# Performance work log

Measured on AMD Instinct MI355X. Metric: run time of the kernel, lower is better.

The kernel has to match this reference:

```python
import jax, jax.numpy as jnp
import numpy as np

B, N = 16, 286
EMB_DIM = 4
CLOUD_DIM = 4
NB = 3          # number_of_basis
HID = 150       # radial MLP hidden width
RADIUS = 3.0    # neighbor radius / max_radius of cosine basis
FF = 512


def sp5(x):
    # torch Softplus(beta=5)
    return jax.nn.softplus(5.0 * x) / 5.0


def cosine_basis(r):
    # e3nn CosineBasisModel embedding: cos^2 bumps on [0, RADIUS]
    centers = jnp.linspace(0.0, RADIUS, NB)
    step = centers[1] - centers[0]
    d = (r[..., None] - centers) / step                     # [B,N,N,NB]
    return jnp.cos(jnp.pi / 2 * d) ** 2 * (jnp.abs(d) < 1.0)


def cloud_conv(feats, dist, mask, ws, bs, dim_out):
    # radial MLP on pairwise distances -> per-pair [dim_out, dim_in] kernel (l=0 only)
    x = cosine_basis(dist)
    for w, b in zip(ws[:-1], bs[:-1]):
        x = sp5(x @ w + b)
    R = x @ ws[-1] + bs[-1]                                 # [B,N,N,dim_out*dim_in]
    b_, n_ = dist.shape[0], dist.shape[1]
    k = R.reshape(b_, n_, n_, dim_out, -1) * mask[..., None, None]
    nb = jnp.maximum(mask.sum(-1), 1.0)                     # neighbors per atom [B,N]
    out = jnp.einsum('zabij,zbj->zai', k, feats) / jnp.sqrt(nb)[..., None]
    return out


def setup_inputs() -> dict:
    key = jax.random.key(0)
    ks = jax.random.split(key, 32)
    xyz = jax.random.normal(ks[0], (B, N, 3), dtype=jnp.float32)
    Z = jax.random.randint(ks[1], (B, N), 0, 11)
    emb = jax.random.normal(ks[2], (11, EMB_DIM), dtype=jnp.float32)
    inp = {'xyz': xyz, 'Z': Z, 'emb': emb}
    # radial MLPs per cloud: 3 -> 150 -> 150 -> 150 -> dim_out*dim_in (=16)
    dims = [NB, HID, HID, HID, CLOUD_DIM * CLOUD_DIM]
    ki = 3
    for c in range(2):
        for l in range(4):
            w = jax.random.normal(ks[ki], (dims[l], dims[l + 1]), dtype=jnp.float32) / np.sqrt(dims[l])
            b = jnp.zeros((dims[l + 1],), dtype=jnp.float32)
            inp[f'c{c}_w{l}'] = w
            inp[f'c{c}_b{l}'] = b
            ki += 1
    cloud_out = CLOUD_DIM * 2  # cloud_dim * cloud_order^2 * nclouds = 8
    inp['fc_w'] = jax.random.normal(ks[ki], (cloud_out, FF), dtype=jnp.float32) / np.sqrt(cloud_out); ki += 1
    inp['fc_b'] = jnp.zeros((FF,), dtype=jnp.float32)
    inp['bn_g'] = jnp.ones((FF,), dtype=jnp.float32)
    inp['bn_b'] = jnp.zeros((FF,), dtype=jnp.float32)
    inp['out_w'] = jax.random.normal(ks[ki], (FF, 1), dtype=jnp.float32) / np.sqrt(FF); ki += 1
    inp['out_b'] = jnp.zeros((1,), dtype=jnp.float32)
    return inp


def reference(xyz, Z, emb,
              c0_w0, c0_b0, c0_w1, c0_b1, c0_w2, c0_b2, c0_w3, c0_b3,
              c1_w0, c1_b0, c1_w1, c1_b1, c1_w2, c1_b2, c1_w3, c1_b3,
              fc_w, fc_b, bn_g, bn_b, out_w, out_b):
    feats = emb[Z]                                          # [B,N,emb_dim]
    diff = xyz[:, :, None, :] - xyz[:, None, :, :]
    dist = jnp.sqrt(jnp.sum(diff * diff, -1) + 1e-12)       # [B,N,N]
    mask = (dist < RADIUS).astype(feats.dtype)
    f1 = cloud_conv(feats, dist, mask,
                    [c0_w0, c0_w1, c0_w2, c0_w3], [c0_b0, c0_b1, c0_b2, c0_b3], CLOUD_DIM)
    f2 = cloud_conv(f1, dist, mask,
                    [c1_w0, c1_w1, c1_w2, c1_w3], [c1_b0, c1_b1, c1_b2, c1_b3], CLOUD_DIM)
    feats_cat = jnp.concatenate([f1, f2], axis=2)           # [B,N,8]
    # lp_pool2d(norm=2, kernel=(N,1)) == L2 norm over atom dim
    pooled = jnp.sqrt(jnp.sum(feats_cat ** 2, axis=1))      # [B,8]
    h = jax.nn.softplus(pooled @ fc_w + fc_b)
    mean = h.mean(0)
    var = h.var(0)
    h = jax.nn.softplus((h - mean) / jnp.sqrt(var + 1e-5) * bn_g + bn_b)
    return jax.nn.sigmoid(h @ out_w + out_b)[:, 0]          # [B]
```

## Files before the change

kernel.cpp:

```cpp
#include <hip/hip_runtime.h>
#include <hip/hip_bf16.h>
#include <hip/hip_fp16.h>
#include <math.h>

#define B_SZ   16
#define N_ATOM 286
#define NT     1024
#define HIDW   150
#define FF_DIM 512
#define WPAD   152
#define WROWS  151

__device__ __forceinline__ float softplus_f(float x) {
  return fmaxf(x, 0.0f) + log1pf(expf(-fabsf(x)));
}
__device__ __forceinline__ float sp5_f(float x) {
  float t = 5.0f * x;
  return (fmaxf(t, 0.0f) + log1pf(expf(-fabsf(t)))) * 0.2f;
}

__global__ __launch_bounds__(256) void prep_kernel(
    const float* __restrict__ w1a, const float* __restrict__ b1a,
    const float* __restrict__ w2a, const float* __restrict__ b2a,
    const float* __restrict__ w1c, const float* __restrict__ b1c,
    const float* __restrict__ w2c, const float* __restrict__ b2c,
    float* __restrict__ Wp) {
  const int m = blockIdx.y;
  const float* W  = (m == 0) ? w1a : (m == 1) ? w2a : (m == 2) ? w1c : w2c;
  const float* Bb = (m == 0) ? b1a : (m == 1) ? b2a : (m == 2) ? b1c : b2c;
  int idx = blockIdx.x * 256 + threadIdx.x;
  if (idx < WROWS * WPAD) {
    int i = idx / WPAD, o = idx % WPAD;
    float v = 0.0f;
    if (o < HIDW) v = (i < HIDW) ? W[i * HIDW + o] : Bb[o];
    Wp[(size_t)m * WROWS * WPAD + idx] = v;
  }
}

__device__ __forceinline__ void hidden_layer_v2(
    const float* __restrict__ Wp,
    const float* __restrict__ src,
    float* __restrict__ dst,
    int jj, int e0) {
  const float4 bb = *(const float4*)(Wp + HIDW * WPAD + 4 * jj);
  float4 a0 = bb, a1 = bb;
  #pragma unroll 8
  for (int i = 0; i < HIDW; ++i) {
    float4 wv = *(const float4*)(Wp + i * WPAD + 4 * jj);
    float2 h  = *(const float2*)(src + i * 8 + e0);
    a0.x = __builtin_fmaf(h.x, wv.x, a0.x); a1.x = __builtin_fmaf(h.y, wv.x, a1.x);
    a0.y = __builtin_fmaf(h.x, wv.y, a0.y); a1.y = __builtin_fmaf(h.y, wv.y, a1.y);
    a0.z = __builtin_fmaf(h.x, wv.z, a0.z); a1.z = __builtin_fmaf(h.y, wv.z, a1.z);
    a0.w = __builtin_fmaf(h.x, wv.w, a0.w); a1.w = __builtin_fmaf(h.y, wv.w, a1.w);
  }
  *(float2*)(dst + (4 * jj + 0) * 8 + e0) = make_float2(sp5_f(a0.x), sp5_f(a1.x));
  *(float2*)(dst + (4 * jj + 1) * 8 + e0) = make_float2(sp5_f(a0.y), sp5_f(a1.y));
  *(float2*)(dst + (4 * jj + 2) * 8 + e0) = make_float2(sp5_f(a0.z), sp5_f(a1.z));
  *(float2*)(dst + (4 * jj + 3) * 8 + e0) = make_float2(sp5_f(a0.w), sp5_f(a1.w));
}

__global__ __launch_bounds__(256) void table_kernel(
    const float* __restrict__ a_w0, const float* __restrict__ a_b0,
    const float* __restrict__ a_w3, const float* __restrict__ a_b3,
    const float* __restrict__ c_w0, const float* __restrict__ c_b0,
    const float* __restrict__ c_w3, const float* __restrict__ c_b3,
    const float* __restrict__ Wp,
    __half* __restrict__ tabh0, __half* __restrict__ tabh1) {
  __shared__ float actA[WPAD * 8];
  __shared__ float actB[WPAD * 8];

  const int nblk = NT / 8;
  const int cloud = (blockIdx.x >= nblk) ? 1 : 0;
  const int blk   = blockIdx.x - cloud * nblk;
  const float* w0 = cloud ? c_w0 : a_w0;  const float* b0 = cloud ? c_b0 : a_b0;
  const float* w3 = cloud ? c_w3 : a_w3;  const float* b3 = cloud ? c_b3 : a_b3;
  const float* Wp1 = Wp + (size_t)(cloud * 2)     * WROWS * WPAD;
  const float* Wp2 = Wp + (size_t)(cloud * 2 + 1) * WROWS * WPAD;
  __half* table = cloud ? tabh1 : tabh0;

  const int tid  = threadIdx.x;
  const int lane = tid & 63;
  const int wave = __builtin_amdgcn_readfirstlane(tid >> 6);
  const int e0   = wave * 2;
  const int gbase = blk * 8;
  const int jj = (lane < 38) ? lane : 37;

  float x0[3], x1[3];
  #pragma unroll
  for (int k = 0; k < 3; ++k) {
    float r0 = 3.0f * (float)(gbase + e0)     / (float)(NT - 1);
    float r1 = 3.0f * (float)(gbase + e0 + 1) / (float)(NT - 1);
    float d0 = (r0 - 1.5f * (float)k) * (1.0f / 1.5f);
    float d1 = (r1 - 1.5f * (float)k) * (1.0f / 1.5f);
    float c0 = cosf(1.57079632679489662f * d0);
    float c1 = cosf(1.57079632679489662f * d1);
    x0[k] = (fabsf(d0) < 1.0f) ? c0 * c0 : 0.0f;
    x1[k] = (fabsf(d1) < 1.0f) ? c1 * c1 : 0.0f;
  }

  #pragma unroll
  for (int c = 0; c < 3; ++c) {
    int o = lane + 64 * c;
    int oc = (o < HIDW) ? o : (HIDW - 1);
    float w00 = w0[oc], w01 = w0[HIDW + oc], w02 = w0[2 * HIDW + oc], bb = b0[oc];
    float h0 = sp5_f(bb + x0[0] * w00 + x0[1] * w01 + x0[2] * w02);
    float h1 = sp5_f(bb + x1[0] * w00 + x1[1] * w01 + x1[2] * w02);
    if (o < HIDW) *(float2*)(actA + o * 8 + e0) = make_float2(h0, h1);
  }

  hidden_layer_v2(Wp1, actA, actB, jj, e0);
  hidden_layer_v2(Wp2, actB, actA, jj, e0);

  {
    const int o  = lane & 15;
    const int ig = lane >> 4;
    float a0 = 0.f, a1 = 0.f;
    for (int i = ig; i < HIDW; i += 4) {
      float wv = w3[i * 16 + o];
      float h0 = actA[i * 8 + e0];
      float h1 = actA[i * 8 + e0 + 1];
      a0 = __builtin_fmaf(h0, wv, a0);
      a1 = __builtin_fmaf(h1, wv, a1);
    }
    a0 += __shfl_xor(a0, 16, 64); a0 += __shfl_xor(a0, 32, 64);
    a1 += __shfl_xor(a1, 16, 64); a1 += __shfl_xor(a1, 32, 64);
    if (lane < 16) {
      float bb = b3[o];
      table[(size_t)(gbase + e0)     * 16 + o] = __float2half(a0 + bb);
      table[(size_t)(gbase + e0 + 1) * 16 + o] = __float2half(a1 + bb);
    }
  }
}

__device__ __forceinline__ void cvt8(uint4 q, float* out) {
  const __half2* h = (const __half2*)&q;
  #pragma unroll
  for (int k = 0; k < 4; ++k) {
    float2 f = __half22float2(h[k]);
    out[2 * k] = f.x; out[2 * k + 1] = f.y;
  }
}

__global__ __launch_bounds__(256) void conv_kernel(
    const float* __restrict__ xyz, const int* __restrict__ Z,
    const float* __restrict__ emb, const float* __restrict__ feats_in,
    const __half* __restrict__ tabh, float* __restrict__ f_out, int gather) {
  const int wave = threadIdx.x >> 6;
  const int lane = threadIdx.x & 63;
  const int row = blockIdx.x * 4 + wave;
  if (row >= B_SZ * N_ATOM) return;
  const int z = row / N_ATOM, a = row % N_ATOM;
  const float* xz = xyz + (size_t)z * N_ATOM * 3;
  const float ax = xz[a * 3 + 0], ay = xz[a * 3 + 1], az = xz[a * 3 + 2];

  float acc[4] = {0.f, 0.f, 0.f, 0.f};
  float cnt = 0.f;
  for (int b = lane; b < N_ATOM; b += 64) {
    float bx = xz[b * 3 + 0], by = xz[b * 3 + 1], bz = xz[b * 3 + 2];
    float dx = ax - bx, dy = ay - by, dz = az - bz;
    float r = sqrtf(dx * dx + dy * dy + dz * dz + 1e-12f);
    if (r < 3.0f) {
      cnt += 1.0f;
      float t = r * ((float)(NT - 1) / 3.0f);
      int idx = (int)t;
      if (idx > NT - 2) idx = NT - 2;
      float fr = t - (float)idx;
      const uint4* Tp = (const uint4*)(tabh + (size_t)idx * 16);
      uint4 q0 = Tp[0], q1 = Tp[1], q2 = Tp[2], q3 = Tp[3];
      float4 fb;
      if (gather) {
        int zi = Z[z * N_ATOM + b];
        fb = *(const float4*)(emb + (size_t)zi * 4);
      } else {
        fb = *(const float4*)(feats_in + ((size_t)z * N_ATOM + b) * 4);
      }
      float r0[16], r1[16];
      cvt8(q0, r0); cvt8(q1, r0 + 8);
      cvt8(q2, r1); cvt8(q3, r1 + 8);
      #pragma unroll
      for (int i = 0; i < 4; ++i) {
        float v0 = r0[4 * i + 0] + fr * (r1[4 * i + 0] - r0[4 * i + 0]);
        float v1 = r0[4 * i + 1] + fr * (r1[4 * i + 1] - r0[4 * i + 1]);
        float v2 = r0[4 * i + 2] + fr * (r1[4 * i + 2] - r0[4 * i + 2]);
        float v3 = r0[4 * i + 3] + fr * (r1[4 * i + 3] - r0[4 * i + 3]);
        acc[i] += v0 * fb.x + v1 * fb.y + v2 * fb.z + v3 * fb.w;
      }
    }
  }
  #pragma unroll
  for (int m = 32; m > 0; m >>= 1) {
    #pragma unroll
    for (int i = 0; i < 4; ++i) acc[i] += __shfl_xor(acc[i], m, 64);
    cnt += __shfl_xor(cnt, m, 64);
  }
  if (lane == 0) {
    float nb = cnt < 1.0f ? 1.0f : cnt;
    float sc = 1.0f / sqrtf(nb);
    float4 o;
    o.x = acc[0] * sc; o.y = acc[1] * sc; o.z = acc[2] * sc; o.w = acc[3] * sc;
    *(float4*)(f_out + (size_t)row * 4) = o;
  }
}

__global__ __launch_bounds__(512) void tail_kernel(
    const float* __restrict__ f1, const float* __restrict__ f2,
    const float* __restrict__ fc_w, const float* __restrict__ fc_b,
    const float* __restrict__ bn_g, const float* __restrict__ bn_b,
    const float* __restrict__ out_w, const float* __restrict__ out_b,
    float* __restrict__ out) {
  __shared__ float pooled[16][8];
  __shared__ float part[8][16];
  const int tid = threadIdx.x;

  {
    int pair = tid >> 2;
    int sub  = tid & 3;
    int z = pair >> 3, c = pair & 7;
    const float* src = (c < 4) ? f1 : f2;
    int cc = c & 3;
    float s = 0.f;
    for (int a = sub; a < N_ATOM; a += 4) {
      float v = src[((size_t)z * N_ATOM + a) * 4 + cc];
      s += v * v;
    }
    s += __shfl_xor(s, 1, 64);
    s += __shfl_xor(s, 2, 64);
    if (sub == 0) pooled[z][c] = sqrtf(s);
  }
  __syncthreads();

  const int f = tid;
  float hv[16];
  float mean = 0.f;
  #pragma unroll
  for (int z = 0; z < 16; ++z) {
    float a = fc_b[f];
    #pragma unroll
    for (int c = 0; c < 8; ++c) a += pooled[z][c] * fc_w[c * FF_DIM + f];
    hv[z] = softplus_f(a);
    mean += hv[z];
  }
  mean *= (1.0f / 16.0f);
  float var = 0.f;
  #pragma unroll
  for (int z = 0; z < 16; ++z) { float d = hv[z] - mean; var += d * d; }
  var *= (1.0f / 16.0f);
  float istd = 1.0f / sqrtf(var + 1e-5f);
  float g = bn_g[f], bb = bn_b[f], ow = out_w[f];
  float contrib[16];
  #pragma unroll
  for (int z = 0; z < 16; ++z)
    contrib[z] = softplus_f((hv[z] - mean) * istd * g + bb) * ow;

  const int lane = tid & 63, wv = tid >> 6;
  #pragma unroll
  for (int m = 32; m > 0; m >>= 1) {
    #pragma unroll
    for (int z = 0; z < 16; ++z) contrib[z] += __shfl_xor(contrib[z], m, 64);
  }
  if (lane == 0) {
    #pragma unroll
    for (int z = 0; z < 16; ++z) part[wv][z] = contrib[z];
  }
  __syncthreads();
  if (tid < 16) {
    float s = out_b[0];
    #pragma unroll
    for (int w8 = 0; w8 < 8; ++w8) s += part[w8][tid];
    out[tid] = 1.0f / (1.0f + expf(-s));
  }
}

extern "C" void kernel_launch(void* const* d_in, const int* in_sizes, int n_in,
                              void* d_out, int out_size, void* d_ws, size_t ws_size,
                              hipStream_t stream) {
  const float* xyz = (const float*)d_in[0];
  const int*   Z   = (const int*)d_in[1];
  const float* emb = (const float*)d_in[2];
  const float* c0[8]; const float* c1[8];
  for (int i = 0; i < 8; ++i) {
    c0[i] = (const float*)d_in[3 + i];
    c1[i] = (const float*)d_in[11 + i];
  }
  const float* fc_w  = (const float*)d_in[19];
  const float* fc_b  = (const float*)d_in[20];
  const float* bn_g  = (const float*)d_in[21];
  const float* bn_b  = (const float*)d_in[22];
  const float* out_w = (const float*)d_in[23];
  const float* out_b = (const float*)d_in[24];
  float* out = (float*)d_out;

  float* wsf = (float*)d_ws;
  float* Wp = wsf;
  float* f1 = Wp + (size_t)4 * WROWS * WPAD;
  float* f2 = f1 + (size_t)B_SZ * N_ATOM * 4;
  __half* tabh0 = (__half*)(f2 + (size_t)B_SZ * N_ATOM * 4);
  __half* tabh1 = tabh0 + (size_t)NT * 16;

  {
    dim3 g((WROWS * WPAD + 255) / 256, 4);
    prep_kernel<<<g, 256, 0, stream>>>(c0[2], c0[3], c0[4], c0[5],
                                       c1[2], c1[3], c1[4], c1[5], Wp);
  }

  table_kernel<<<2 * (NT / 8), 256, 0, stream>>>(
      c0[0], c0[1], c0[6], c0[7],
      c1[0], c1[1], c1[6], c1[7],
      Wp, tabh0, tabh1);

  const int conv_blocks = (B_SZ * N_ATOM + 3) / 4;
  conv_kernel<<<conv_blocks, 256, 0, stream>>>(xyz, Z, emb, (const float*)nullptr,
                                               tabh0, f1, 1);
  conv_kernel<<<conv_blocks, 256, 0, stream>>>(xyz, Z, emb, f1,
                                               tabh1, f2, 0);

  tail_kernel<<<1, 512, 0, stream>>>(f1, f2, fc_w, fc_b, bn_g, bn_b,
                                     out_w, out_b, out);
}
```

Baseline: 196.7 us.

## Keep MLP activations in registers via wave shuffles; split pooling into parallel kernel

The radial-MLP hidden layers in the table kernel now keep each wave's activations in registers and broadcast them with cross-lane shuffles, instead of staging them through shared memory between layers. This removes the LDS round trips in the two 150x150 layers but adds many shuffle instructions and a fully unrolled loop that raises register pressure. Separately, the L2 pooling over atoms moves out of the single-block tail kernel into a 16-block pool kernel using float4 loads, spreading that reduction across more CUs at the cost of one extra launch.

```diff
diff --git a/kernel.cpp b/kernel.cpp
--- a/kernel.cpp
+++ b/kernel.cpp
@@ -37,26 +37,31 @@
   }
 }
 
-__device__ __forceinline__ void hidden_layer_v2(
+__device__ __forceinline__ void hlayer_shfl(
     const float* __restrict__ Wp,
-    const float* __restrict__ src,
-    float* __restrict__ dst,
-    int jj, int e0) {
+    float4& p0, float4& p1, int jj) {
   const float4 bb = *(const float4*)(Wp + HIDW * WPAD + 4 * jj);
   float4 a0 = bb, a1 = bb;
-  #pragma unroll 8
-  for (int i = 0; i < HIDW; ++i) {
-    float4 wv = *(const float4*)(Wp + i * WPAD + 4 * jj);
-    float2 h  = *(const float2*)(src + i * 8 + e0);
-    a0.x = __builtin_fmaf(h.x, wv.x, a0.x); a1.x = __builtin_fmaf(h.y, wv.x, a1.x);
-    a0.y = __builtin_fmaf(h.x, wv.y, a0.y); a1.y = __builtin_fmaf(h.y, wv.y, a1.y);
-    a0.z = __builtin_fmaf(h.x, wv.z, a0.z); a1.z = __builtin_fmaf(h.y, wv.z, a1.z);
-    a0.w = __builtin_fmaf(h.x, wv.w, a0.w); a1.w = __builtin_fmaf(h.y, wv.w, a1.w);
-  }
-  *(float2*)(dst + (4 * jj + 0) * 8 + e0) = make_float2(sp5_f(a0.x), sp5_f(a1.x));
-  *(float2*)(dst + (4 * jj + 1) * 8 + e0) = make_float2(sp5_f(a0.y), sp5_f(a1.y));
-  *(float2*)(dst + (4 * jj + 2) * 8 + e0) = make_float2(sp5_f(a0.z), sp5_f(a1.z));
-  *(float2*)(dst + (4 * jj + 3) * 8 + e0) = make_float2(sp5_f(a0.w), sp5_f(a1.w));
+  #pragma unroll
+  for (int ii = 0; ii < 38; ++ii) {
+    #pragma unroll
+    for (int c = 0; c < 4; ++c) {
+      const int i = 4 * ii + c;
+      if (i < HIDW) {
+        float4 wv = *(const float4*)(Wp + i * WPAD + 4 * jj);
+        float s0 = (c == 0) ? p0.x : (c == 1) ? p0.y : (c == 2) ? p0.z : p0.w;
+        float s1 = (c == 0) ? p1.x : (c == 1) ? p1.y : (c == 2) ? p1.z : p1.w;
+        float h0 = __shfl(s0, ii, 64);
+        float h1 = __shfl(s1, ii, 64);
+        a0.x = __builtin_fmaf(h0, wv.x, a0.x); a1.x = __builtin_fmaf(h1, wv.x, a1.x);
+        a0.y = __builtin_fmaf(h0, wv.y, a0.y); a1.y = __builtin_fmaf(h1, wv.y, a1.y);
+        a0.z = __builtin_fmaf(h0, wv.z, a0.z); a1.z = __builtin_fmaf(h1, wv.z, a1.z);
+        a0.w = __builtin_fmaf(h0, wv.w, a0.w); a1.w = __builtin_fmaf(h1, wv.w, a1.w);
+      }
+    }
+  }
+  p0 = make_float4(sp5_f(a0.x), sp5_f(a0.y), sp5_f(a0.z), sp5_f(a0.w));
+  p1 = make_float4(sp5_f(a1.x), sp5_f(a1.y), sp5_f(a1.z), sp5_f(a1.w));
 }
 
 __global__ __launch_bounds__(256) void table_kernel(
@@ -66,8 +71,7 @@
     const float* __restrict__ c_w3, const float* __restrict__ c_b3,
     const float* __restrict__ Wp,
     __half* __restrict__ tabh0, __half* __restrict__ tabh1) {
-  __shared__ float actA[WPAD * 8];
-  __shared__ float actB[WPAD * 8];
+  __shared__ float actA[HIDW * 8];
 
   const int nblk = NT / 8;
   const int cloud = (blockIdx.x >= nblk) ? 1 : 0;
@@ -98,18 +102,35 @@
     x1[k] = (fabsf(d1) < 1.0f) ? c1 * c1 : 0.0f;
   }
 
-  #pragma unroll
-  for (int c = 0; c < 3; ++c) {
-    int o = lane + 64 * c;
-    int oc = (o < HIDW) ? o : (HIDW - 1);
-    float w00 = w0[oc], w01 = w0[HIDW + oc], w02 = w0[2 * HIDW + oc], bb = b0[oc];
-    float h0 = sp5_f(bb + x0[0] * w00 + x0[1] * w01 + x0[2] * w02);
-    float h1 = sp5_f(bb + x1[0] * w00 + x1[1] * w01 + x1[2] * w02);
-    if (o < HIDW) *(float2*)(actA + o * 8 + e0) = make_float2(h0, h1);
-  }
-
-  hidden_layer_v2(Wp1, actA, actB, jj, e0);
-  hidden_layer_v2(Wp2, actB, actA, jj, e0);
+  float4 p0, p1;
+  {
+    float v0[4], v1[4];
+    #pragma unroll
+    for (int c = 0; c < 4; ++c) {
+      int o = 4 * jj + c;
+      int oc = (o < HIDW) ? o : (HIDW - 1);
+      float w00 = w0[oc], w01 = w0[HIDW + oc], w02 = w0[2 * HIDW + oc];
+      float bb = b0[oc];
+      v0[c] = sp5_f(bb + x0[0] * w00 + x0[1] * w01 + x0[2] * w02);
+      v1[c] = sp5_f(bb + x1[0] * w00 + x1[1] * w01 + x1[2] * w02);
+    }
+    p0 = make_float4(v0[0], v0[1], v0[2], v0[3]);
+    p1 = make_float4(v1[0], v1[1], v1[2], v1[3]);
+  }
+
+  hlayer_shfl(Wp1, p0, p1, jj);
+  hlayer_shfl(Wp2, p0, p1, jj);
+
+  {
+    float v0[4] = {p0.x, p0.y, p0.z, p0.w};
+    float v1[4] = {p1.x, p1.y, p1.z, p1.w};
+    #pragma unroll
+    for (int c = 0; c < 4; ++c) {
+      int o = 4 * jj + c;
+      if (o < HIDW) *(float2*)(actA + o * 8 + e0) = make_float2(v0[c], v1[c]);
+    }
+  }
+  __syncthreads();
 
   {
     const int o  = lane & 15;
@@ -202,8 +223,38 @@
   }
 }
 
+__global__ __launch_bounds__(256) void pool_kernel(
+    const float* __restrict__ f1, const float* __restrict__ f2,
+    float* __restrict__ pool_sq) {
+  __shared__ float red[4][8];
+  const int z = blockIdx.x;
+  const int tid = threadIdx.x;
+  const int lane = tid & 63, wave = tid >> 6;
+  float s[8] = {0.f, 0.f, 0.f, 0.f, 0.f, 0.f, 0.f, 0.f};
+  for (int a = tid; a < N_ATOM; a += 256) {
+    float4 v1 = *(const float4*)(f1 + ((size_t)z * N_ATOM + a) * 4);
+    float4 v2 = *(const float4*)(f2 + ((size_t)z * N_ATOM + a) * 4);
+    s[0] += v1.x * v1.x; s[1] += v1.y * v1.y;
+    s[2] += v1.z * v1.z; s[3] += v1.w * v1.w;
+    s[4] += v2.x * v2.x; s[5] += v2.y * v2.y;
+    s[6] += v2.z * v2.z; s[7] += v2.w * v2.w;
+  }
+  #pragma unroll
+  for (int m = 32; m > 0; m >>= 1) {
+    #pragma unroll
+    for (int k = 0; k < 8; ++k) s[k] += __shfl_xor(s[k], m, 64);
+  }
+  if (lane == 0) {
+    #pragma unroll
+    for (int k = 0; k < 8; ++k) red[wave][k] = s[k];
+  }
+  __syncthreads();
+  if (tid < 8)
+    pool_sq[z * 8 + tid] = red[0][tid] + red[1][tid] + red[2][tid] + red[3][tid];
+}
+
 __global__ __launch_bounds__(512) void tail_kernel(
-    const float* __restrict__ f1, const float* __restrict__ f2,
+    const float* __restrict__ pool_sq,
     const float* __restrict__ fc_w, const float* __restrict__ fc_b,
     const float* __restrict__ bn_g, const float* __restrict__ bn_b,
     const float* __restrict__ out_w, const float* __restrict__ out_b,
@@ -212,21 +263,7 @@
   __shared__ float part[8][16];
   const int tid = threadIdx.x;
 
-  {
-    int pair = tid >> 2;
-    int sub  = tid & 3;
-    int z = pair >> 3, c = pair & 7;
-    const float* src = (c < 4) ? f1 : f2;
-    int cc = c & 3;
-    float s = 0.f;
-    for (int a = sub; a < N_ATOM; a += 4) {
-      float v = src[((size_t)z * N_ATOM + a) * 4 + cc];
-      s += v * v;
-    }
-    s += __shfl_xor(s, 1, 64);
-    s += __shfl_xor(s, 2, 64);
-    if (sub == 0) pooled[z][c] = sqrtf(s);
-  }
+  if (tid < 128) pooled[tid >> 3][tid & 7] = sqrtf(pool_sq[tid]);
   __syncthreads();
 
   const int f = tid;
@@ -294,7 +331,8 @@
   float* Wp = wsf;
   float* f1 = Wp + (size_t)4 * WROWS * WPAD;
   float* f2 = f1 + (size_t)B_SZ * N_ATOM * 4;
-  __half* tabh0 = (__half*)(f2 + (size_t)B_SZ * N_ATOM * 4);
+  float* pool_sq = f2 + (size_t)B_SZ * N_ATOM * 4;
+  __half* tabh0 = (__half*)(pool_sq + 128);
   __half* tabh1 = tabh0 + (size_t)NT * 16;
 
   {
@@ -314,6 +352,8 @@
   conv_kernel<<<conv_blocks, 256, 0, stream>>>(xyz, Z, emb, f1,
                                                tabh1, f2, 0);
 
-  tail_kernel<<<1, 512, 0, stream>>>(f1, f2, fc_w, fc_b, bn_g, bn_b,
+  pool_kernel<<<B_SZ, 256, 0, stream>>>(f1, f2, pool_sq);
+
+  tail_kernel<<<1, 512, 0, stream>>>(pool_sq, fc_w, fc_b, bn_g, bn_b,
                                      out_w, out_b, out);
 }
```

Result: slower. 540.0 us (+174.5%).
